# Kernel optimization log

Measured on AMD Instinct MI355X. Metric: run time of the kernel, lower is better.

## Reference

```python
import jax, jax.numpy as jnp
import numpy as np

NUM_EXPERTS = 8
TOP_K = 2


def setup_inputs() -> dict:
    key = jax.random.key(0)
    ks = jax.random.split(key, 6)
    B, S, D, F, E = 2, 2048, 512, 1536, NUM_EXPERTS
    scale = 0.02
    return {
        "x": jax.random.normal(ks[0], (B, S, D), dtype=jnp.float32),
        "Wg": jax.random.normal(ks[1], (D, E), dtype=jnp.float32) * scale,
        "W1": jax.random.normal(ks[2], (E, D, F), dtype=jnp.float32) * scale,
        "W2": jax.random.normal(ks[3], (E, F, D), dtype=jnp.float32) * scale,
        "W3": jax.random.normal(ks[4], (E, D, F), dtype=jnp.float32) * scale,
        "b3": jax.random.normal(ks[5], (E, F), dtype=jnp.float32) * scale,
    }


def reference(x, Wg, W1, W2, W3, b3):
    # Router (eval mode: no noise). x: [B,S,D]
    logits = jnp.einsum("bsd,de->bse", x, Wg)  # [B,S,E]
    top_logits, top_idx = jax.lax.top_k(logits, TOP_K)  # [B,S,K]
    top_w = jax.nn.softmax(top_logits, axis=-1)  # [B,S,K]
    # Combine weights per expert: scatter top-k weights into E slots.
    onehot = jax.nn.one_hot(top_idx, NUM_EXPERTS, dtype=x.dtype)  # [B,S,K,E]
    C = jnp.sum(onehot * top_w[..., None], axis=-2)  # [B,S,E]
    # Dense per-expert SwiGLU FFN; non-selected experts contribute weight 0,
    # so the math matches the original masked gather/scatter exactly.
    h = jnp.einsum("bsd,edf->bsef", x, W1)  # [B,S,E,F]
    g = jnp.einsum("bsd,edf->bsef", x, W3) + b3  # [B,S,E,F]
    act = jax.nn.silu(h) * g  # [B,S,E,F]
    out = jnp.einsum("bse,bsef,efd->bsd", C, act, W2)  # [B,S,D]
    return out
```

## Files before the change

### kernel.cpp

```cpp
#include <hip/hip_runtime.h>

constexpr int NTOK = 4096;
constexpr int DIM  = 512;
constexpr int FF   = 1536;
constexpr int NE   = 8;

typedef __attribute__((ext_vector_type(8))) short short8;
typedef __attribute__((ext_vector_type(4))) float f32x4;

static __device__ __forceinline__ unsigned short f2bf(float f) {
    unsigned int x = __float_as_uint(f);
    unsigned int r = x + 0x7fffu + ((x >> 16) & 1u);
    return (unsigned short)(r >> 16);
}

static __device__ __forceinline__ void gload_lds16(const void* g, void* l) {
    __builtin_amdgcn_global_load_lds(
        (const __attribute__((address_space(1))) unsigned int*)g,
        (__attribute__((address_space(3))) unsigned int*)l, 16, 0, 0);
}

__global__ __launch_bounds__(256) void moe_router(
    const float* __restrict__ x, const float* __restrict__ wg,
    int* __restrict__ eidx, float* __restrict__ wts, unsigned short* __restrict__ xbf)
{
    int lane = threadIdx.x & 63;
    int wave = threadIdx.x >> 6;
    int tok  = blockIdx.x * 4 + wave;

    float acc[NE];
#pragma unroll
    for (int e = 0; e < NE; ++e) acc[e] = 0.f;

    const float* xr = x + (size_t)tok * DIM;
    unsigned short* xo = xbf + (size_t)tok * DIM;
#pragma unroll
    for (int i = 0; i < DIM / 64; ++i) {
        int d = i * 64 + lane;
        float xv = xr[d];
        xo[d] = f2bf(xv);
        const float4* wr = (const float4*)(wg + (size_t)d * NE);
        float4 w0 = wr[0], w1 = wr[1];
        acc[0] += xv * w0.x; acc[1] += xv * w0.y; acc[2] += xv * w0.z; acc[3] += xv * w0.w;
        acc[4] += xv * w1.x; acc[5] += xv * w1.y; acc[6] += xv * w1.z; acc[7] += xv * w1.w;
    }
#pragma unroll
    for (int e = 0; e < NE; ++e) {
#pragma unroll
        for (int off = 32; off >= 1; off >>= 1)
            acc[e] += __shfl_xor(acc[e], off, 64);
    }
    if (lane == 0) {
        int i0 = 0; float m0 = acc[0];
#pragma unroll
        for (int e = 1; e < NE; ++e) if (acc[e] > m0) { m0 = acc[e]; i0 = e; }
        int i1 = -1; float m1 = -3.4e38f;
#pragma unroll
        for (int e = 0; e < NE; ++e) if (e != i0 && acc[e] > m1) { m1 = acc[e]; i1 = e; }
        float e1 = expf(m1 - m0);
        float s  = 1.f + e1;
        int s0 = tok * 2, s1 = tok * 2 + 1;
        wts[s0] = 1.f / s;
        wts[s1] = e1 / s;
        eidx[s0] = i0;
        eidx[s1] = i1;
    }
}

__global__ __launch_bounds__(256) void moe_count(
    const int* __restrict__ eidx, int* __restrict__ pcnt)
{
    __shared__ int s_wc[4][8];
    int tid = threadIdx.x, lane = tid & 63, wv = tid >> 6;
    int e = eidx[blockIdx.x * 256 + tid];
#pragma unroll
    for (int e0 = 0; e0 < 8; ++e0) {
        unsigned long long bal = __ballot(e == e0);
        if (lane == 0) s_wc[wv][e0] = __popcll(bal);
    }
    __syncthreads();
    if (tid < 8)
        pcnt[blockIdx.x * 8 + tid] = s_wc[0][tid] + s_wc[1][tid] + s_wc[2][tid] + s_wc[3][tid];
}

__global__ __launch_bounds__(256) void moe_scatter(
    const int* __restrict__ eidx, const int* __restrict__ pcnt,
    int* __restrict__ clist, int* __restrict__ cnt, int* __restrict__ ebase)
{
    __shared__ int s_all[256];
    __shared__ int s_wc[4][8];
    int tid = threadIdx.x, bx = blockIdx.x;
    int lane = tid & 63, wv = tid >> 6;
    s_all[tid] = pcnt[tid];
    int slot = bx * 256 + tid;
    int e = eidx[slot];
    int myoff = 0;
#pragma unroll
    for (int e0 = 0; e0 < 8; ++e0) {
        unsigned long long bal = __ballot(e == e0);
        if (lane == 0) s_wc[wv][e0] = __popcll(bal);
        if (e == e0) myoff = __popcll(bal & ((1ull << lane) - 1ull));
    }
    __syncthreads();
    int base = 0;
#pragma unroll
    for (int ep = 0; ep < 8; ++ep) {
        int t = 0;
        for (int b = 0; b < 32; ++b) t += s_all[b * 8 + ep];
        if (ep < e) base += (t + 7) & ~7;
    }
    int cbase = 0;
    for (int b = 0; b < bx; ++b) cbase += s_all[b * 8 + e];
    int wbase = 0;
    for (int w = 0; w < wv; ++w) wbase += s_wc[w][e];
    clist[base + cbase + wbase + myoff] = slot;
    if (bx == 0 && tid == 0) {
        int eb = 0;
        for (int ep = 0; ep < 8; ++ep) {
            int t = 0;
            for (int b = 0; b < 32; ++b) t += s_all[b * 8 + ep];
            cnt[ep] = t;
            ebase[ep] = eb;
            eb += (t + 7) & ~7;
        }
    }
}

__global__ __launch_bounds__(256) void transpose_cvt2(
    const float* __restrict__ inA, unsigned short* __restrict__ outA,
    const float* __restrict__ inB, unsigned short* __restrict__ outB,
    int R, int C)
{
    __shared__ float tile[64][65];
    int c0 = blockIdx.x * 64, r0 = blockIdx.y * 64, z = blockIdx.z;
    const float* in      = (z < 8) ? inA  : inB;
    unsigned short* out  = (z < 8) ? outA : outB;
    int zz = z & 7;
    const float* ip = in + (size_t)zz * R * C;
    char* op = (char*)(out + (size_t)zz * R * C);

    int tr = threadIdx.x >> 4;
    int tc = (threadIdx.x & 15) * 4;
#pragma unroll
    for (int p = 0; p < 4; ++p) {
        int r = p * 16 + tr;
        float4 v = *(const float4*)(ip + (size_t)(r0 + r) * C + c0 + tc);
        tile[r][tc + 0] = v.x; tile[r][tc + 1] = v.y;
        tile[r][tc + 2] = v.z; tile[r][tc + 3] = v.w;
    }
    __syncthreads();
#pragma unroll
    for (int p = 0; p < 4; ++p) {
        int c = p * 16 + tr;
        ushort4 o;
        o.x = f2bf(tile[tc + 0][c]);
        o.y = f2bf(tile[tc + 1][c]);
        o.z = f2bf(tile[tc + 2][c]);
        o.w = f2bf(tile[tc + 3][c]);
        int cb = ((r0 + tc) * 2) ^ ((c & 7) << 4);
        *(ushort4*)(op + (size_t)(c0 + c) * (R * 2) + cb) = o;
    }
}

__global__ __launch_bounds__(256, 2) void moe_ffn1(
    const unsigned short* __restrict__ xbf,
    const unsigned short* __restrict__ w1t,
    const unsigned short* __restrict__ w3t,
    const float* __restrict__ b3,
    const int* __restrict__ cnt, const int* __restrict__ ebase,
    const int* __restrict__ clist,
    unsigned short* __restrict__ actc)
{
    int e    = blockIdx.y >> 5;
    int mb   = blockIdx.y & 31;
    int n0   = blockIdx.x * 128;
    int ce   = cnt[e];
    int row0 = mb * 128;
    if (row0 >= ce) return;
    int eb   = ebase[e];

    __shared__ __attribute__((aligned(16))) char smem[49152];
    __shared__ int s_slot[128];
    char* sA  = smem;
    char* sB1 = smem + 16384;
    char* sB3 = smem + 32768;

    int tid = threadIdx.x;
    if (tid < 128) {
        int r = row0 + tid;
        s_slot[tid] = (r < ce) ? clist[eb + r] : clist[eb + row0];
    }
    __syncthreads();

    int lane = tid & 63, wv = tid >> 6;
    int wm = wv >> 1, wn = wv & 1;
    int lrow = lane >> 3;
    int lcol = (lane & 7) * 16;
    int aswz = lcol ^ (lrow << 4);

    const char* aSrc[4]; const char* b1Src[4]; const char* b3Src[4];
#pragma unroll
    for (int i = 0; i < 4; ++i) {
        int rr = i * 32 + wv * 8 + lrow;
        aSrc[i] = (const char*)xbf + (size_t)(s_slot[rr] >> 1) * (DIM * 2) + aswz;
        size_t rb = ((size_t)e * FF + n0 + rr) * (DIM * 2) + lcol;
        b1Src[i] = (const char*)w1t + rb;
        b3Src[i] = (const char*)w3t + rb;
    }

    f32x4 acch[4][4], accg[4][4];
#pragma unroll
    for (int i = 0; i < 4; ++i)
#pragma unroll
        for (int j = 0; j < 4; ++j) { acch[i][j] = (f32x4)0.f; accg[i][j] = (f32x4)0.f; }

    for (int kc = 0; kc < DIM * 2; kc += 128) {
#pragma unroll
        for (int i = 0; i < 4; ++i) {
            int ro = (i * 32 + wv * 8) * 128;
            gload_lds16(aSrc[i]  + kc, sA  + ro);
            gload_lds16(b1Src[i] + kc, sB1 + ro);
            gload_lds16(b3Src[i] + kc, sB3 + ro);
        }
        __syncthreads();

#pragma unroll
        for (int ks = 0; ks < 2; ++ks) {
            short8 af[4], b1f[4], b3f[4];
#pragma unroll
            for (int mi = 0; mi < 4; ++mi) {
                int row = wm * 64 + mi * 16 + (lane & 15);
                int ba  = row * 128 + ((ks * 64 + (lane >> 4) * 16) ^ ((row & 7) << 4));
                af[mi] = *(const short8*)(sA + ba);
            }
#pragma unroll
            for (int ni = 0; ni < 4; ++ni) {
                int row = wn * 64 + ni * 16 + (lane & 15);
                int ba  = row * 128 + ((ks * 64 + (lane >> 4) * 16) ^ ((row & 7) << 4));
                b1f[ni] = *(const short8*)(sB1 + ba);
                b3f[ni] = *(const short8*)(sB3 + ba);
            }
#pragma unroll
            for (int mi = 0; mi < 4; ++mi)
#pragma unroll
                for (int ni = 0; ni < 4; ++ni) {
                    acch[mi][ni] = __builtin_amdgcn_mfma_f32_16x16x32_bf16(af[mi], b1f[ni], acch[mi][ni], 0, 0, 0);
                    accg[mi][ni] = __builtin_amdgcn_mfma_f32_16x16x32_bf16(af[mi], b3f[ni], accg[mi][ni], 0, 0, 0);
                }
        }
        __syncthreads();
    }

    char* sE = smem;
#pragma unroll
    for (int ni = 0; ni < 4; ++ni) {
        int col = wn * 64 + ni * 16 + (lane & 15);
        float b3v = b3[e * FF + n0 + col];
#pragma unroll
        for (int mi = 0; mi < 4; ++mi) {
            int rbase = wm * 64 + mi * 16 + (lane >> 4) * 4;
#pragma unroll
            for (int r = 0; r < 4; ++r) {
                float h = acch[mi][ni][r];
                float g = accg[mi][ni][r] + b3v;
                float a = (h / (1.f + __expf(-h))) * g;
                *(unsigned short*)(sE + (rbase + r) * 256 + col * 2) = f2bf(a);
            }
        }
    }
    __syncthreads();

    int lim = ce - row0;
#pragma unroll
    for (int it = 0; it < 8; ++it) {
        int chunk = it * 256 + tid;
        int row = chunk >> 4, c8 = chunk & 15;
        if (row < lim) {
            int crow = eb + row0 + row;
            size_t dst = (size_t)crow * (FF * 2) + n0 * 2 + ((c8 * 16) ^ ((crow & 7) << 4));
            *(short8*)((char*)actc + dst) = *(const short8*)(sE + row * 256 + c8 * 16);
        }
    }
}

__global__ __launch_bounds__(256) void moe_ffn2(
    const unsigned short* __restrict__ actc,
    const unsigned short* __restrict__ w2t,
    const int* __restrict__ cnt, const int* __restrict__ ebase,
    const int* __restrict__ clist, const float* __restrict__ wts,
    float* __restrict__ yws)
{
    int e    = blockIdx.y >> 5;
    int mb   = blockIdx.y & 31;
    int n0   = blockIdx.x * 64;
    int ce   = cnt[e];
    int row0 = mb * 128;
    if (row0 >= ce) return;
    int eb   = ebase[e];

    __shared__ __attribute__((aligned(16))) char smem[32768];
    __shared__ int   s_slot[128];
    __shared__ float s_w[128];
    char* sA = smem;
    char* sB = smem + 16384;

    int tid = threadIdx.x;
    if (tid < 128) {
        int r  = row0 + tid;
        int sl = (r < ce) ? clist[eb + r] : clist[eb + row0];
        s_slot[tid] = sl;
        s_w[tid]    = wts[sl];
    }
    __syncthreads();

    int lane = tid & 63, wv = tid >> 6;
    int wm = wv >> 1, wn = wv & 1;
    int lrow = lane >> 3;
    int lcol = (lane & 7) * 16;

    const char* aSrc[4];
#pragma unroll
    for (int i = 0; i < 4; ++i) {
        int rr = i * 32 + wv * 8 + lrow;
        int cr = (row0 + rr < ce) ? (eb + row0 + rr) : (eb + row0);
        aSrc[i] = (const char*)actc + (size_t)cr * (FF * 2) + lcol;
    }
    const char* bSrc[2];
#pragma unroll
    for (int i = 0; i < 2; ++i) {
        int rr = i * 32 + wv * 8 + lrow;
        bSrc[i] = (const char*)w2t + ((size_t)e * DIM + n0 + rr) * (FF * 2) + lcol;
    }

    f32x4 acc[4][2];
#pragma unroll
    for (int i = 0; i < 4; ++i)
#pragma unroll
        for (int j = 0; j < 2; ++j) acc[i][j] = (f32x4)0.f;

    for (int kc = 0; kc < FF * 2; kc += 128) {
#pragma unroll
        for (int i = 0; i < 4; ++i)
            gload_lds16(aSrc[i] + kc, sA + (i * 32 + wv * 8) * 128);
#pragma unroll
        for (int i = 0; i < 2; ++i)
            gload_lds16(bSrc[i] + kc, sB + (i * 32 + wv * 8) * 128);
        __syncthreads();

#pragma unroll
        for (int ks = 0; ks < 2; ++ks) {
            short8 af[4], bf[2];
#pragma unroll
            for (int mi = 0; mi < 4; ++mi) {
                int row = wm * 64 + mi * 16 + (lane & 15);
                int ba  = row * 128 + ((ks * 64 + (lane >> 4) * 16) ^ ((row & 7) << 4));
                af[mi] = *(const short8*)(sA + ba);
            }
#pragma unroll
            for (int ni = 0; ni < 2; ++ni) {
                int row = wn * 32 + ni * 16 + (lane & 15);
                int ba  = row * 128 + ((ks * 64 + (lane >> 4) * 16) ^ ((row & 7) << 4));
                bf[ni] = *(const short8*)(sB + ba);
            }
#pragma unroll
            for (int mi = 0; mi < 4; ++mi)
#pragma unroll
                for (int ni = 0; ni < 2; ++ni)
                    acc[mi][ni] = __builtin_amdgcn_mfma_f32_16x16x32_bf16(af[mi], bf[ni], acc[mi][ni], 0, 0, 0);
        }
        __syncthreads();
    }

    char* sE = smem;
#pragma unroll
    for (int mi = 0; mi < 4; ++mi) {
        int rbase = wm * 64 + mi * 16 + (lane >> 4) * 4;
#pragma unroll
        for (int r = 0; r < 4; ++r) {
            int row = rbase + r;
            float w = s_w[row];
#pragma unroll
            for (int ni = 0; ni < 2; ++ni) {
                int col = wn * 32 + ni * 16 + (lane & 15);
                *(float*)(sE + row * 256 + col * 4) = acc[mi][ni][r] * w;
            }
        }
    }
    __syncthreads();

    int lim = ce - row0;
#pragma unroll
    for (int it = 0; it < 8; ++it) {
        int chunk = it * 256 + tid;
        int row = chunk >> 4, c4 = chunk & 15;
        if (row < lim)
            *(float4*)(yws + (size_t)s_slot[row] * DIM + n0 + c4 * 4) =
                *(const float4*)(sE + row * 256 + c4 * 16);
    }
}

__global__ __launch_bounds__(256) void moe_combine(
    const float* __restrict__ yws, float* __restrict__ out)
{
    int i  = blockIdx.x * 256 + threadIdx.x;
    int t  = i >> 7;
    int d4 = (i & 127) * 4;
    const float4* y0 = (const float4*)(yws + ((size_t)(2 * t)     * DIM + d4));
    const float4* y1 = (const float4*)(yws + ((size_t)(2 * t + 1) * DIM + d4));
    float4 a = *y0, b = *y1;
    float4 o = make_float4(a.x + b.x, a.y + b.y, a.z + b.z, a.w + b.w);
    *(float4*)(out + (size_t)t * DIM + d4) = o;
}

extern "C" void kernel_launch(void* const* d_in, const int* in_sizes, int n_in,
                              void* d_out, int out_size, void* d_ws, size_t ws_size,
                              hipStream_t stream)
{
    const float* x  = (const float*)d_in[0];
    const float* wg = (const float*)d_in[1];
    const float* w1 = (const float*)d_in[2];
    const float* w2 = (const float*)d_in[3];
    const float* w3 = (const float*)d_in[4];
    const float* b3 = (const float*)d_in[5];
    float* out = (float*)d_out;
    char*  ws  = (char*)d_ws;

    int*   cnt   = (int*)(ws + 0);
    int*   ebase = (int*)(ws + 64);
    int*   pcnt  = (int*)(ws + 256);
    int*   eidx  = (int*)(ws + 2048);
    float* wts   = (float*)(ws + 2048 + 32768);
    int*   clist = (int*)(ws + 2048 + 65536);
    constexpr size_t OFF_BIG = 102400;
    constexpr size_t WB = (size_t)NE * DIM * FF * 2;
    unsigned short* w2t  = (unsigned short*)(ws + OFF_BIG);
    unsigned short* w1t  = (unsigned short*)(ws + OFF_BIG + WB);
    unsigned short* w3t  = (unsigned short*)(ws + OFF_BIG + 2 * WB);
    unsigned short* actc = (unsigned short*)(ws + OFF_BIG + 3 * WB);
    unsigned short* xbf  = w2t;
    float*          yws  = (float*)w1t;

    moe_router <<<NTOK / 4, 256, 0, stream>>>(x, wg, eidx, wts, xbf);
    moe_count  <<<32, 256, 0, stream>>>(eidx, pcnt);
    moe_scatter<<<32, 256, 0, stream>>>(eidx, pcnt, clist, cnt, ebase);

    dim3 tgA(FF / 64, DIM / 64, 16);
    transpose_cvt2<<<tgA, 256, 0, stream>>>(w1, w1t, w3, w3t, DIM, FF);

    dim3 g1(FF / 128, NE * 32);
    moe_ffn1<<<g1, 256, 0, stream>>>(xbf, w1t, w3t, b3, cnt, ebase, clist, actc);

    dim3 tgB(DIM / 64, FF / 64, 8);
    transpose_cvt2<<<tgB, 256, 0, stream>>>(w2, w2t, w2, w2t, FF, DIM);

    dim3 g2(DIM / 64, NE * 32);
    moe_ffn2<<<g2, 256, 0, stream>>>(actc, w2t, cnt, ebase, clist, wts, yws);

    moe_combine<<<(NTOK * DIM / 4) / 256, 256, 0, stream>>>(yws, out);
}
```

Before: 222.8 us.

## Fuse combine into ffn2 via atomics and interleave experts in 1D grids

```diff
diff --git a/kernel.cpp b/kernel.cpp
--- a/kernel.cpp
+++ b/kernel.cpp
@@ -162,7 +162,7 @@
     }
 }
 
-__global__ __launch_bounds__(256, 2) void moe_ffn1(
+__global__ __launch_bounds__(256, 3) void moe_ffn1(
     const unsigned short* __restrict__ xbf,
     const unsigned short* __restrict__ w1t,
     const unsigned short* __restrict__ w3t,
@@ -171,9 +171,11 @@
     const int* __restrict__ clist,
     unsigned short* __restrict__ actc)
 {
-    int e    = blockIdx.y >> 5;
-    int mb   = blockIdx.y & 31;
-    int n0   = blockIdx.x * 128;
+    int p    = blockIdx.x;
+    int e    = p & 7;
+    int q    = p >> 3;
+    int mb   = q / 12;
+    int n0   = (q - mb * 12) * 128;
     int ce   = cnt[e];
     int row0 = mb * 128;
     if (row0 >= ce) return;
@@ -288,17 +290,19 @@
     const unsigned short* __restrict__ w2t,
     const int* __restrict__ cnt, const int* __restrict__ ebase,
     const int* __restrict__ clist, const float* __restrict__ wts,
-    float* __restrict__ yws)
-{
-    int e    = blockIdx.y >> 5;
-    int mb   = blockIdx.y & 31;
-    int n0   = blockIdx.x * 64;
+    float* __restrict__ out)
+{
+    int p    = blockIdx.x;
+    int e    = p & 7;
+    int q    = p >> 3;
+    int mb   = q >> 3;
+    int n0   = (q & 7) * 64;
     int ce   = cnt[e];
     int row0 = mb * 128;
     if (row0 >= ce) return;
     int eb   = ebase[e];
 
-    __shared__ __attribute__((aligned(16))) char smem[32768];
+    __shared__ __attribute__((aligned(16))) char smem[24576];
     __shared__ int   s_slot[128];
     __shared__ float s_w[128];
     char* sA = smem;
@@ -371,45 +375,22 @@
         __syncthreads();
     }
 
-    char* sE = smem;
 #pragma unroll
     for (int mi = 0; mi < 4; ++mi) {
-        int rbase = wm * 64 + mi * 16 + (lane >> 4) * 4;
 #pragma unroll
         for (int r = 0; r < 4; ++r) {
-            int row = rbase + r;
-            float w = s_w[row];
-#pragma unroll
-            for (int ni = 0; ni < 2; ++ni) {
-                int col = wn * 32 + ni * 16 + (lane & 15);
-                *(float*)(sE + row * 256 + col * 4) = acc[mi][ni][r] * w;
-            }
-        }
-    }
-    __syncthreads();
-
-    int lim = ce - row0;
-#pragma unroll
-    for (int it = 0; it < 8; ++it) {
-        int chunk = it * 256 + tid;
-        int row = chunk >> 4, c4 = chunk & 15;
-        if (row < lim)
-            *(float4*)(yws + (size_t)s_slot[row] * DIM + n0 + c4 * 4) =
-                *(const float4*)(sE + row * 256 + c4 * 16);
-    }
-}
-
-__global__ __launch_bounds__(256) void moe_combine(
-    const float* __restrict__ yws, float* __restrict__ out)
-{
-    int i  = blockIdx.x * 256 + threadIdx.x;
-    int t  = i >> 7;
-    int d4 = (i & 127) * 4;
-    const float4* y0 = (const float4*)(yws + ((size_t)(2 * t)     * DIM + d4));
-    const float4* y1 = (const float4*)(yws + ((size_t)(2 * t + 1) * DIM + d4));
-    float4 a = *y0, b = *y1;
-    float4 o = make_float4(a.x + b.x, a.y + b.y, a.z + b.z, a.w + b.w);
-    *(float4*)(out + (size_t)t * DIM + d4) = o;
+            int rg = wm * 64 + mi * 16 + (lane >> 4) * 4 + r;
+            if (row0 + rg < ce) {
+                float w   = s_w[rg];
+                int   tok = s_slot[rg] >> 1;
+#pragma unroll
+                for (int ni = 0; ni < 2; ++ni) {
+                    int dd = n0 + wn * 32 + ni * 16 + (lane & 15);
+                    atomicAdd(&out[(size_t)tok * DIM + dd], acc[mi][ni][r] * w);
+                }
+            }
+        }
+    }
 }
 
 extern "C" void kernel_launch(void* const* d_in, const int* in_sizes, int n_in,
@@ -438,7 +419,8 @@
     unsigned short* w3t  = (unsigned short*)(ws + OFF_BIG + 2 * WB);
     unsigned short* actc = (unsigned short*)(ws + OFF_BIG + 3 * WB);
     unsigned short* xbf  = w2t;
-    float*          yws  = (float*)w1t;
+
+    hipMemsetAsync(out, 0, (size_t)NTOK * DIM * sizeof(float), stream);
 
     moe_router <<<NTOK / 4, 256, 0, stream>>>(x, wg, eidx, wts, xbf);
     moe_count  <<<32, 256, 0, stream>>>(eidx, pcnt);
@@ -447,14 +429,10 @@
     dim3 tgA(FF / 64, DIM / 64, 16);
     transpose_cvt2<<<tgA, 256, 0, stream>>>(w1, w1t, w3, w3t, DIM, FF);
 
-    dim3 g1(FF / 128, NE * 32);
-    moe_ffn1<<<g1, 256, 0, stream>>>(xbf, w1t, w3t, b3, cnt, ebase, clist, actc);
+    moe_ffn1<<<NE * 32 * 12, 256, 0, stream>>>(xbf, w1t, w3t, b3, cnt, ebase, clist, actc);
 
     dim3 tgB(DIM / 64, FF / 64, 8);
     transpose_cvt2<<<tgB, 256, 0, stream>>>(w2, w2t, w2, w2t, FF, DIM);
 
-    dim3 g2(DIM / 64, NE * 32);
-    moe_ffn2<<<g2, 256, 0, stream>>>(actc, w2t, cnt, ebase, clist, wts, yws);
-
-    moe_combine<<<(NTOK * DIM / 4) / 256, 256, 0, stream>>>(yws, out);
-}
+    moe_ffn2<<<NE * 32 * 8, 256, 0, stream>>>(actc, w2t, cnt, ebase, clist, wts, out);
+}
```

New measurement: 275.7 us. 1.24x slower.
